# Optimization experiments

Hardware: AMD Instinct MI355X
Metric: run time of the kernel (lower is better)

Reference implementation:

```python
import jax, jax.numpy as jnp
import numpy as np

GROUP = 128  # int4 quant group size and Hadamard block size

# Sylvester Hadamard matrix of size 128, orthonormal (H @ H.T = I)
_h = np.array([[1.0]], dtype=np.float32)
while _h.shape[0] < GROUP:
    _h = np.kron(_h, np.array([[1.0, 1.0], [1.0, -1.0]], dtype=np.float32))
H128 = jnp.asarray(_h / np.sqrt(GROUP))


def hadamard_rotate(x):
    # blockwise Hadamard rotation along the last dim (last dim % 128 == 0)
    *lead, n = x.shape
    xr = x.reshape(*lead, n // GROUP, GROUP) @ H128
    return xr.reshape(*lead, n)


def dequant_int4(wq, scales):
    # wq: [out, in] uint4 values in [0,16); scales: [out, in//GROUP]
    out_dim, in_dim = wq.shape
    w = (wq.astype(jnp.float32) - 8.0).reshape(out_dim, in_dim // GROUP, GROUP)
    w = w * scales[:, :, None]
    return w.reshape(out_dim, in_dim)


def rotate_linear_int4(x, wq, scales):
    # y = hadamard(x) @ dequant(W).T
    return hadamard_rotate(x) @ dequant_int4(wq, scales).T


def setup_inputs() -> dict:
    key = jax.random.key(0)
    ks = jax.random.split(key, 7)
    T, D, I = 4096, 4096, 12288  # tokens, hidden, intermediate
    x = jax.random.normal(ks[0], (T, D), dtype=jnp.float32)
    wq_gate = jax.random.randint(ks[1], (I, D), 0, 16, dtype=jnp.int32)
    s_gate = jax.random.uniform(ks[2], (I, D // GROUP), dtype=jnp.float32) * 0.01
    wq_up = jax.random.randint(ks[3], (I, D), 0, 16, dtype=jnp.int32)
    s_up = jax.random.uniform(ks[4], (I, D // GROUP), dtype=jnp.float32) * 0.01
    wq_down = jax.random.randint(ks[5], (D, I), 0, 16, dtype=jnp.int32)
    s_down = jax.random.uniform(ks[6], (D, I // GROUP), dtype=jnp.float32) * 0.01
    return {"x": x, "wq_gate": wq_gate, "s_gate": s_gate,
            "wq_up": wq_up, "s_up": s_up,
            "wq_down": wq_down, "s_down": s_down}


def reference(x, wq_gate, s_gate, wq_up, s_up, wq_down, s_down):
    gate = rotate_linear_int4(x, wq_gate, s_gate)   # [T, I]
    up = rotate_linear_int4(x, wq_up, s_up)         # [T, I]
    h = jax.nn.silu(gate) * up                       # SiluAndMul on cat([gate, up])
    return rotate_linear_int4(h, wq_down, s_down)    # [T, D]
```

## Files before the change

kernel.cpp:

```cpp
#include <hip/hip_runtime.h>
#include <hip/hip_bf16.h>
#include <cstdint>

#define T_DIM 4096
#define D_DIM 4096
#define I_DIM 12288
#define GRP   128

typedef __attribute__((ext_vector_type(8))) short bf16x8;
typedef __attribute__((ext_vector_type(4))) float f32x4;
typedef __attribute__((ext_vector_type(4))) int   int32x4;

typedef __attribute__((address_space(3))) void lds_void;
typedef const __attribute__((address_space(1))) void gmem_void;

static __device__ __forceinline__ unsigned short f2bf(float f) {
    unsigned int u = __float_as_uint(f);
    u += 0x7FFFu + ((u >> 16) & 1u);
    return (unsigned short)(u >> 16);
}
static __device__ __forceinline__ float bf2f(unsigned short b) {
    return __uint_as_float(((unsigned int)b) << 16);
}

__global__ void had_f32_to_bf16(const float* __restrict__ in, unsigned short* __restrict__ out,
                                int ngroups) {
    int gid = blockIdx.x * (blockDim.x >> 6) + (threadIdx.x >> 6);
    if (gid >= ngroups) return;
    int lane = threadIdx.x & 63;
    const float2 v2 = *reinterpret_cast<const float2*>(in + (size_t)gid * 128 + lane * 2);
    float v0 = v2.x, v1 = v2.y;
    { float t0 = v0 + v1, t1 = v0 - v1; v0 = t0; v1 = t1; }
#pragma unroll
    for (int m = 1; m <= 32; m <<= 1) {
        float b0 = __shfl_xor(v0, m);
        float b1 = __shfl_xor(v1, m);
        if (lane & m) { v0 = b0 - v0; v1 = b1 - v1; }
        else          { v0 = v0 + b0; v1 = v1 + b1; }
    }
    const float s = 0.08838834764831843f;
    unsigned int o = (unsigned int)f2bf(v0 * s) | ((unsigned int)f2bf(v1 * s) << 16);
    *reinterpret_cast<unsigned int*>(out + (size_t)gid * 128 + lane * 2) = o;
}

__global__ void had_bf16_inplace(unsigned short* __restrict__ buf, int ngroups) {
    int gid = blockIdx.x * (blockDim.x >> 6) + (threadIdx.x >> 6);
    if (gid >= ngroups) return;
    int lane = threadIdx.x & 63;
    unsigned int pv = *reinterpret_cast<const unsigned int*>(buf + (size_t)gid * 128 + lane * 2);
    float v0 = __uint_as_float((pv & 0xFFFFu) << 16);
    float v1 = __uint_as_float(pv & 0xFFFF0000u);
    { float t0 = v0 + v1, t1 = v0 - v1; v0 = t0; v1 = t1; }
#pragma unroll
    for (int m = 1; m <= 32; m <<= 1) {
        float b0 = __shfl_xor(v0, m);
        float b1 = __shfl_xor(v1, m);
        if (lane & m) { v0 = b0 - v0; v1 = b1 - v1; }
        else          { v0 = v0 + b0; v1 = v1 + b1; }
    }
    const float s = 0.08838834764831843f;
    unsigned int o = (unsigned int)f2bf(v0 * s) | ((unsigned int)f2bf(v1 * s) << 16);
    *reinterpret_cast<unsigned int*>(buf + (size_t)gid * 128 + lane * 2) = o;
}

__global__ void dequant_w(const int* __restrict__ Wq, const float* __restrict__ S,
                          unsigned short* __restrict__ Wbf, int In, int total8) {
    int t = blockIdx.x * blockDim.x + threadIdx.x;
    if (t >= total8) return;
    size_t base = (size_t)t * 8;
    size_t row = base / (size_t)In;
    int col = (int)(base - row * (size_t)In);
    float sc = S[row * (size_t)(In >> 7) + (col >> 7)];
    const int32x4* p = reinterpret_cast<const int32x4*>(Wq + base);
    int32x4 a = p[0], b = p[1];
    float nsc = -8.0f * sc;
    unsigned int o0 = (unsigned int)f2bf((float)a.x * sc + nsc) |
                      ((unsigned int)f2bf((float)a.y * sc + nsc) << 16);
    unsigned int o1 = (unsigned int)f2bf((float)a.z * sc + nsc) |
                      ((unsigned int)f2bf((float)a.w * sc + nsc) << 16);
    unsigned int o2 = (unsigned int)f2bf((float)b.x * sc + nsc) |
                      ((unsigned int)f2bf((float)b.y * sc + nsc) << 16);
    unsigned int o3 = (unsigned int)f2bf((float)b.z * sc + nsc) |
                      ((unsigned int)f2bf((float)b.w * sc + nsc) << 16);
    *reinterpret_cast<uint4*>(Wbf + base) = make_uint4(o0, o1, o2, o3);
}


#define GBAR()  __builtin_amdgcn_s_barrier()
#define LGKM0() asm volatile("s_waitcnt lgkmcnt(0)" ::: "memory")
#define VM4()   asm volatile("s_waitcnt vmcnt(4)" ::: "memory")
#define VM0()   asm volatile("s_waitcnt vmcnt(0)" ::: "memory")

#define STAGE(bb, s, kb)                                                               \
  { const int kh_ = (s) >> 1;                                                          \
    const unsigned short* src_ = ((s) & 1) ? W : A;                                    \
    const int row0_ = ((s) & 1) ? n0 : m0;                                             \
    _Pragma("unroll")                                                                  \
    for (int i_ = 0; i_ < 2; ++i_) {                                                   \
      int j_ = i_ * 512 + tid;                                                         \
      int row_ = j_ >> 2;                                                              \
      int gs_ = (tid & 3) ^ ((row_ >> 1) & 3);                                         \
      const unsigned short* gp_ = src_ + (size_t)(row0_ + row_) * K + (kb) + kh_ * 32 + gs_ * 8; \
      unsigned short* lp_ = lds + ((bb) << 15) + (((s) & 1) << 14) + (kh_ << 13)       \
                            + (i_ * 512 + (wid << 6)) * 8;                             \
      __builtin_amdgcn_global_load_lds((gmem_void*)gp_, (lds_void*)lp_, 16, 0, 0);     \
    } }

#define LOADA(bb, kh, mg)                                                              \
  _Pragma("unroll")                                                                    \
  for (int mi_ = 0; mi_ < 4; ++mi_) {                                                  \
    int row_ = (wr << 7) + ((mg) * 4 + mi_) * 16 + (lane & 15);                        \
    af[mi_] = *reinterpret_cast<const bf16x8*>(lds + ((bb) << 15) + ((kh) << 13)       \
              + row_ * 32 + ((kc ^ ((row_ >> 1) & 3)) << 3));                          \
  }

#define LOADB(bb, kh)                                                                  \
  _Pragma("unroll")                                                                    \
  for (int ni_ = 0; ni_ < 4; ++ni_) {                                                  \
    int nr_ = (wc << 6) + ni_ * 16 + (lane & 15);                                      \
    bk[ni_] = *reinterpret_cast<const bf16x8*>(lds + ((bb) << 15) + 16384              \
              + ((kh) << 13) + nr_ * 32 + ((kc ^ ((nr_ >> 1) & 3)) << 3));             \
  }

#define MFMA16(mg)                                                                     \
  _Pragma("unroll")                                                                    \
  for (int mi_ = 0; mi_ < 4; ++mi_)                                                    \
  _Pragma("unroll")                                                                    \
  for (int ni_ = 0; ni_ < 4; ++ni_)                                                    \
    acc[(mg) * 4 + mi_][ni_] =                                                         \
      __builtin_amdgcn_mfma_f32_16x16x32_bf16(af[mi_], bk[ni_], acc[(mg) * 4 + mi_][ni_], 0, 0, 0);

template<int MODE>
__global__ __launch_bounds__(512, 2)
void gemm256(const unsigned short* __restrict__ A,
             const unsigned short* __restrict__ W,
             void* __restrict__ C, int M, int N, int K)
{
    __shared__ __align__(16) unsigned short lds[65536];

    const int MT = M >> 8;
    const int nwg = gridDim.x;
    const int bid = blockIdx.x;
    const int cpx = nwg >> 3;
    const int wg  = (bid & 7) * cpx + (bid >> 3);
    const int m0 = (wg % MT) << 8;
    const int n0 = (wg / MT) << 8;

    const int tid  = threadIdx.x;
    const int lane = tid & 63;
    const int wid  = tid >> 6;
    const int wr = wid >> 2;
    const int wc = wid & 3;
    const int kc = lane >> 4;

    f32x4 acc[8][4];
#pragma unroll
    for (int i = 0; i < 8; ++i)
#pragma unroll
        for (int j = 0; j < 4; ++j) acc[i][j] = (f32x4)0.0f;

    const int NT = K >> 6;

    STAGE(0, 0, 0); STAGE(0, 1, 0); STAGE(0, 2, 0); STAGE(0, 3, 0);
    VM4();
    GBAR();

    for (int kt = 0; kt < NT; ++kt) {
        const int b  = kt & 1;
        const int kn = (kt + 1) << 6;
        const bool st = (kt + 1 < NT);
        bf16x8 af[4], bk[4];

        LOADB(b, 0); LOADA(b, 0, 0);
        if (st) STAGE(b ^ 1, 0, kn);
        GBAR(); LGKM0();
        __builtin_amdgcn_s_setprio(1); MFMA16(0); __builtin_amdgcn_s_setprio(0);
        GBAR();
        LOADA(b, 0, 1);
        if (st) STAGE(b ^ 1, 1, kn);
        GBAR(); LGKM0();
        __builtin_amdgcn_s_setprio(1); MFMA16(1); __builtin_amdgcn_s_setprio(0);
        if (st) { VM4(); } else { VM0(); }
        GBAR();
        LOADB(b, 1); LOADA(b, 1, 0);
        if (st) STAGE(b ^ 1, 2, kn);
        GBAR(); LGKM0();
        __builtin_amdgcn_s_setprio(1); MFMA16(0); __builtin_amdgcn_s_setprio(0);
        GBAR();
        LOADA(b, 1, 1);
        if (st) STAGE(b ^ 1, 3, kn);
        GBAR(); LGKM0();
        __builtin_amdgcn_s_setprio(1); MFMA16(1); __builtin_amdgcn_s_setprio(0);
        if (st) { VM4(); }
        GBAR();
    }

#pragma unroll
    for (int mi = 0; mi < 8; ++mi)
#pragma unroll
        for (int ni = 0; ni < 4; ++ni) {
            const int col = n0 + (wc << 6) + ni * 16 + (lane & 15);
#pragma unroll
            for (int r = 0; r < 4; ++r) {
                const int row = m0 + (wr << 7) + mi * 16 + ((lane >> 4) << 2) + r;
                const size_t idx = (size_t)row * N + col;
                if (MODE == 2) {
                    ((float*)C)[idx] = acc[mi][ni][r];
                } else if (MODE == 0) {
                    ((unsigned short*)C)[idx] = f2bf(acc[mi][ni][r]);
                } else {
                    float g = bf2f(((unsigned short*)C)[idx]);
                    float u = acc[mi][ni][r];
                    float h = (g / (1.0f + __expf(-g))) * u;
                    ((unsigned short*)C)[idx] = f2bf(h);
                }
            }
        }
}

__global__ __launch_bounds__(256, 2)
void gemm_gateup_fb(const unsigned short* __restrict__ Xr,
                    const int* __restrict__ Wg, const float* __restrict__ Sg,
                    const int* __restrict__ Wu, const float* __restrict__ Su,
                    unsigned short* __restrict__ H)
{
    __shared__ __align__(16) unsigned short lA [128 * 64];
    __shared__ __align__(16) unsigned short lBg[128 * 64];
    __shared__ __align__(16) unsigned short lBu[128 * 64];
    const int MT = T_DIM / 128;
    const int bid = blockIdx.x;
    const int m0 = (bid % MT) * 128;
    const int n0 = (bid / MT) * 128;
    const int tid  = threadIdx.x;
    const int lane = tid & 63;
    const int wid  = tid >> 6;
    const int wr = wid >> 1, wc = wid & 1;
    f32x4 accG[4][4], accU[4][4];
#pragma unroll
    for (int i = 0; i < 4; ++i)
#pragma unroll
        for (int j = 0; j < 4; ++j) { accG[i][j] = (f32x4)0.0f; accU[i][j] = (f32x4)0.0f; }
    const int arow = lane >> 3;
    const int acol = (lane & 7) * 8;
    const int SStride = D_DIM / GRP;
    for (int k0 = 0; k0 < D_DIM; k0 += 64) {
        __syncthreads();
#pragma unroll
        for (int it = 0; it < 4; ++it) {
            int chunk = wid * 4 + it;
            const unsigned short* gp = Xr + (size_t)(m0 + chunk * 8 + arow) * D_DIM + k0 + acol;
            __builtin_amdgcn_global_load_lds((gmem_void*)gp, (lds_void*)(lA + chunk * 512), 16, 0, 0);
        }
        const int g = k0 >> 7;
#pragma unroll
        for (int i = 0; i < 8; ++i) {
            int linear = i * 1024 + tid * 4;
            int r = linear >> 6;
            int c = linear & 63;
            const int32x4 wg = *reinterpret_cast<const int32x4*>(Wg + (size_t)(n0 + r) * D_DIM + k0 + c);
            const int32x4 wu = *reinterpret_cast<const int32x4*>(Wu + (size_t)(n0 + r) * D_DIM + k0 + c);
            float scg = Sg[(size_t)(n0 + r) * SStride + g];
            float scu = Su[(size_t)(n0 + r) * SStride + g];
            unsigned int g01 = (unsigned int)f2bf((float)(wg.x - 8) * scg) | ((unsigned int)f2bf((float)(wg.y - 8) * scg) << 16);
            unsigned int g23 = (unsigned int)f2bf((float)(wg.z - 8) * scg) | ((unsigned int)f2bf((float)(wg.w - 8) * scg) << 16);
            unsigned int u01 = (unsigned int)f2bf((float)(wu.x - 8) * scu) | ((unsigned int)f2bf((float)(wu.y - 8) * scu) << 16);
            unsigned int u23 = (unsigned int)f2bf((float)(wu.z - 8) * scu) | ((unsigned int)f2bf((float)(wu.w - 8) * scu) << 16);
            *reinterpret_cast<uint2*>(lBg + r * 64 + c) = make_uint2(g01, g23);
            *reinterpret_cast<uint2*>(lBu + r * 64 + c) = make_uint2(u01, u23);
        }
        __syncthreads();
#pragma unroll
        for (int ks = 0; ks < 2; ++ks) {
            const int koff = ks * 32 + (lane >> 4) * 8;
            bf16x8 af[4], bg[4], bu[4];
#pragma unroll
            for (int mi = 0; mi < 4; ++mi)
                af[mi] = *reinterpret_cast<const bf16x8*>(lA + (wr * 64 + mi * 16 + (lane & 15)) * 64 + koff);
#pragma unroll
            for (int ni = 0; ni < 4; ++ni) {
                bg[ni] = *reinterpret_cast<const bf16x8*>(lBg + (wc * 64 + ni * 16 + (lane & 15)) * 64 + koff);
                bu[ni] = *reinterpret_cast<const bf16x8*>(lBu + (wc * 64 + ni * 16 + (lane & 15)) * 64 + koff);
            }
#pragma unroll
            for (int mi = 0; mi < 4; ++mi)
#pragma unroll
                for (int ni = 0; ni < 4; ++ni) {
                    accG[mi][ni] = __builtin_amdgcn_mfma_f32_16x16x32_bf16(af[mi], bg[ni], accG[mi][ni], 0, 0, 0);
                    accU[mi][ni] = __builtin_amdgcn_mfma_f32_16x16x32_bf16(af[mi], bu[ni], accU[mi][ni], 0, 0, 0);
                }
        }
    }
#pragma unroll
    for (int mi = 0; mi < 4; ++mi)
#pragma unroll
        for (int ni = 0; ni < 4; ++ni) {
            const int col = n0 + wc * 64 + ni * 16 + (lane & 15);
#pragma unroll
            for (int r = 0; r < 4; ++r) {
                const int row = m0 + wr * 64 + mi * 16 + (lane >> 4) * 4 + r;
                float gv = accG[mi][ni][r];
                float uv = accU[mi][ni][r];
                float hv = (gv / (1.0f + __expf(-gv))) * uv;
                H[(size_t)row * I_DIM + col] = f2bf(hv);
            }
        }
}

__global__ __launch_bounds__(256, 2)
void gemm_down_fb(const unsigned short* __restrict__ Hr,
                  const int* __restrict__ Wd, const float* __restrict__ Sd,
                  float* __restrict__ Out)
{
    __shared__ __align__(16) unsigned short lA[128 * 64];
    __shared__ __align__(16) unsigned short lB[128 * 64];
    const int MT = T_DIM / 128;
    const int bid = blockIdx.x;
    const int m0 = (bid % MT) * 128;
    const int n0 = (bid / MT) * 128;
    const int tid  = threadIdx.x;
    const int lane = tid & 63;
    const int wid  = tid >> 6;
    const int wr = wid >> 1, wc = wid & 1;
    f32x4 acc[4][4];
#pragma unroll
    for (int i = 0; i < 4; ++i)
#pragma unroll
        for (int j = 0; j < 4; ++j) acc[i][j] = (f32x4)0.0f;
    const int arow = lane >> 3;
    const int acol = (lane & 7) * 8;
    const int SStride = I_DIM / GRP;
    for (int k0 = 0; k0 < I_DIM; k0 += 64) {
        __syncthreads();
#pragma unroll
        for (int it = 0; it < 4; ++it) {
            int chunk = wid * 4 + it;
            const unsigned short* gp = Hr + (size_t)(m0 + chunk * 8 + arow) * I_DIM + k0 + acol;
            __builtin_amdgcn_global_load_lds((gmem_void*)gp, (lds_void*)(lA + chunk * 512), 16, 0, 0);
        }
        const int g = k0 >> 7;
#pragma unroll
        for (int i = 0; i < 8; ++i) {
            int linear = i * 1024 + tid * 4;
            int r = linear >> 6;
            int c = linear & 63;
            const int32x4 wd = *reinterpret_cast<const int32x4*>(Wd + (size_t)(n0 + r) * I_DIM + k0 + c);
            float sc = Sd[(size_t)(n0 + r) * SStride + g];
            unsigned int d01 = (unsigned int)f2bf((float)(wd.x - 8) * sc) | ((unsigned int)f2bf((float)(wd.y - 8) * sc) << 16);
            unsigned int d23 = (unsigned int)f2bf((float)(wd.z - 8) * sc) | ((unsigned int)f2bf((float)(wd.w - 8) * sc) << 16);
            *reinterpret_cast<uint2*>(lB + r * 64 + c) = make_uint2(d01, d23);
        }
        __syncthreads();
#pragma unroll
        for (int ks = 0; ks < 2; ++ks) {
            const int koff = ks * 32 + (lane >> 4) * 8;
            bf16x8 af[4], bfr[4];
#pragma unroll
            for (int mi = 0; mi < 4; ++mi)
                af[mi] = *reinterpret_cast<const bf16x8*>(lA + (wr * 64 + mi * 16 + (lane & 15)) * 64 + koff);
#pragma unroll
            for (int ni = 0; ni < 4; ++ni)
                bfr[ni] = *reinterpret_cast<const bf16x8*>(lB + (wc * 64 + ni * 16 + (lane & 15)) * 64 + koff);
#pragma unroll
            for (int mi = 0; mi < 4; ++mi)
#pragma unroll
                for (int ni = 0; ni < 4; ++ni)
                    acc[mi][ni] = __builtin_amdgcn_mfma_f32_16x16x32_bf16(af[mi], bfr[ni], acc[mi][ni], 0, 0, 0);
        }
    }
#pragma unroll
    for (int mi = 0; mi < 4; ++mi)
#pragma unroll
        for (int ni = 0; ni < 4; ++ni) {
            const int col = n0 + wc * 64 + ni * 16 + (lane & 15);
#pragma unroll
            for (int r = 0; r < 4; ++r) {
                const int row = m0 + wr * 64 + mi * 16 + (lane >> 4) * 4 + r;
                Out[(size_t)row * D_DIM + col] = acc[mi][ni][r];
            }
        }
}

extern "C" void kernel_launch(void* const* d_in, const int* in_sizes, int n_in,
                              void* d_out, int out_size, void* d_ws, size_t ws_size,
                              hipStream_t stream) {
    const float* x       = (const float*)d_in[0];
    const int*   wq_gate = (const int*)d_in[1];
    const float* s_gate  = (const float*)d_in[2];
    const int*   wq_up   = (const int*)d_in[3];
    const float* s_up    = (const float*)d_in[4];
    const int*   wq_down = (const int*)d_in[5];
    const float* s_down  = (const float*)d_in[6];
    float* out = (float*)d_out;

    const size_t XR_E = (size_t)T_DIM * D_DIM;
    const size_t H_E  = (size_t)T_DIM * I_DIM;
    const size_t W_E  = (size_t)I_DIM * D_DIM;
    const size_t need = (XR_E + H_E + 2 * W_E) * sizeof(unsigned short);

    unsigned short* xr = (unsigned short*)d_ws;
    unsigned short* h  = xr + XR_E;

    {
        int ngroups = (int)(XR_E / 128);
        had_f32_to_bf16<<<dim3(ngroups / 4), dim3(256), 0, stream>>>(x, xr, ngroups);
    }

    if (ws_size >= need) {
        unsigned short* wgbf = h + H_E;
        unsigned short* wubf = wgbf + W_E;
        int total8 = (int)(W_E / 8);
        dequant_w<<<dim3((total8 + 255) / 256), dim3(256), 0, stream>>>(wq_gate, s_gate, wgbf, D_DIM, total8);
        dequant_w<<<dim3((total8 + 255) / 256), dim3(256), 0, stream>>>(wq_up,   s_up,   wubf, D_DIM, total8);
        gemm256<0><<<dim3((T_DIM / 256) * (I_DIM / 256)), dim3(512), 0, stream>>>(
            xr, wgbf, (void*)h, T_DIM, I_DIM, D_DIM);
        gemm256<1><<<dim3((T_DIM / 256) * (I_DIM / 256)), dim3(512), 0, stream>>>(
            xr, wubf, (void*)h, T_DIM, I_DIM, D_DIM);
        {
            int ngroups = (int)(H_E / 128);
            had_bf16_inplace<<<dim3(ngroups / 4), dim3(256), 0, stream>>>(h, ngroups);
        }
        dequant_w<<<dim3((total8 + 255) / 256), dim3(256), 0, stream>>>(wq_down, s_down, wgbf, I_DIM, total8);
        gemm256<2><<<dim3((T_DIM / 256) * (D_DIM / 256)), dim3(512), 0, stream>>>(
            h, wgbf, (void*)out, T_DIM, D_DIM, I_DIM);
    } else {
        gemm_gateup_fb<<<dim3((T_DIM / 128) * (I_DIM / 128)), dim3(256), 0, stream>>>(
            xr, wq_gate, s_gate, wq_up, s_up, h);
        {
            int ngroups = (int)(H_E / 128);
            had_bf16_inplace<<<dim3(ngroups / 4), dim3(256), 0, stream>>>(h, ngroups);
        }
        gemm_down_fb<<<dim3((T_DIM / 128) * (D_DIM / 128)), dim3(256), 0, stream>>>(
            h, wq_down, s_down, out);
    }
}
```

Before: 1.415 ms.

## Restructure GEMM mainloop into 8-phase pipeline with full-width 64-K LDS rows

Changes the LDS tile layout from two 32-wide K halves to a single 64-wide row with an 8-way XOR swizzle. The mainloop is rewritten as an 8-phase schedule per two K tiles: B fragments are loaded once per tile and A in four quarter steps, with staging of the next tiles interleaved at finer granularity. The intent is to hide global-to-LDS loads better and cut LDS read traffic for B. It adds more barriers per tile and a hand-tuned vmcnt sequence that assumes NT is even.

Measured after the change: 1.280 ms. 1.11x faster.

```diff
diff --git a/kernel.cpp b/kernel.cpp
--- a/kernel.cpp
+++ b/kernel.cpp
@@ -88,47 +88,53 @@
 
 #define GBAR()  __builtin_amdgcn_s_barrier()
 #define LGKM0() asm volatile("s_waitcnt lgkmcnt(0)" ::: "memory")
-#define VM4()   asm volatile("s_waitcnt vmcnt(4)" ::: "memory")
-#define VM0()   asm volatile("s_waitcnt vmcnt(0)" ::: "memory")
-
-#define STAGE(bb, s, kb)                                                               \
-  { const int kh_ = (s) >> 1;                                                          \
-    const unsigned short* src_ = ((s) & 1) ? W : A;                                    \
-    const int row0_ = ((s) & 1) ? n0 : m0;                                             \
-    _Pragma("unroll")                                                                  \
+#define VMW(n)  asm volatile("s_waitcnt vmcnt(" #n ")" ::: "memory")
+#define P1()    __builtin_amdgcn_s_setprio(1)
+#define P0()    __builtin_amdgcn_s_setprio(0)
+
+#define STG(bb, mat, h, kb)                                                            \
+  { _Pragma("unroll")                                                                  \
     for (int i_ = 0; i_ < 2; ++i_) {                                                   \
-      int j_ = i_ * 512 + tid;                                                         \
-      int row_ = j_ >> 2;                                                              \
-      int gs_ = (tid & 3) ^ ((row_ >> 1) & 3);                                         \
-      const unsigned short* gp_ = src_ + (size_t)(row0_ + row_) * K + (kb) + kh_ * 32 + gs_ * 8; \
-      unsigned short* lp_ = lds + ((bb) << 15) + (((s) & 1) << 14) + (kh_ << 13)       \
-                            + (i_ * 512 + (wid << 6)) * 8;                             \
+      const int rl_ = (h) * 128 + i_ * 64 + (tid >> 3);                                \
+      const int gs_ = (tid & 7) ^ ((tid >> 3) & 7);                                    \
+      const unsigned short* gp_ = ((mat) ? W : A) +                                    \
+          (size_t)(((mat) ? n0 : m0) + rl_) * K + (kb) + gs_ * 8;                      \
+      unsigned short* lp_ = lds + (bb) * 32768 + (mat) * 16384 +                       \
+          ((h) * 128 + i_ * 64 + wid * 8) * 64;                                        \
       __builtin_amdgcn_global_load_lds((gmem_void*)gp_, (lds_void*)lp_, 16, 0, 0);     \
     } }
 
-#define LOADA(bb, kh, mg)                                                              \
-  _Pragma("unroll")                                                                    \
-  for (int mi_ = 0; mi_ < 4; ++mi_) {                                                  \
-    int row_ = (wr << 7) + ((mg) * 4 + mi_) * 16 + (lane & 15);                        \
-    af[mi_] = *reinterpret_cast<const bf16x8*>(lds + ((bb) << 15) + ((kh) << 13)       \
-              + row_ * 32 + ((kc ^ ((row_ >> 1) & 3)) << 3));                          \
+#define LDA(bb, q)                                                                     \
+  _Pragma("unroll")                                                                    \
+  for (int mi_ = 0; mi_ < 2; ++mi_)                                                    \
+  _Pragma("unroll")                                                                    \
+  for (int ks_ = 0; ks_ < 2; ++ks_) {                                                  \
+    int r_ = wr * 128 + ((q) * 2 + mi_) * 16 + (lane & 15);                            \
+    int c_ = ks_ * 4 + kc;                                                             \
+    af[mi_][ks_] = *reinterpret_cast<const bf16x8*>(                                   \
+        lds + (bb) * 32768 + r_ * 64 + ((c_ ^ (r_ & 7)) << 3));                        \
   }
 
-#define LOADB(bb, kh)                                                                  \
-  _Pragma("unroll")                                                                    \
-  for (int ni_ = 0; ni_ < 4; ++ni_) {                                                  \
-    int nr_ = (wc << 6) + ni_ * 16 + (lane & 15);                                      \
-    bk[ni_] = *reinterpret_cast<const bf16x8*>(lds + ((bb) << 15) + 16384              \
-              + ((kh) << 13) + nr_ * 32 + ((kc ^ ((nr_ >> 1) & 3)) << 3));             \
+#define LDB(bb)                                                                        \
+  _Pragma("unroll")                                                                    \
+  for (int ni_ = 0; ni_ < 4; ++ni_)                                                    \
+  _Pragma("unroll")                                                                    \
+  for (int ks_ = 0; ks_ < 2; ++ks_) {                                                  \
+    int r_ = wc * 64 + ni_ * 16 + (lane & 15);                                         \
+    int c_ = ks_ * 4 + kc;                                                             \
+    bk[ni_][ks_] = *reinterpret_cast<const bf16x8*>(                                   \
+        lds + (bb) * 32768 + 16384 + r_ * 64 + ((c_ ^ (r_ & 7)) << 3));                \
   }
 
-#define MFMA16(mg)                                                                     \
-  _Pragma("unroll")                                                                    \
-  for (int mi_ = 0; mi_ < 4; ++mi_)                                                    \
+#define MF16(q)                                                                        \
+  _Pragma("unroll")                                                                    \
+  for (int ks_ = 0; ks_ < 2; ++ks_)                                                    \
+  _Pragma("unroll")                                                                    \
+  for (int mi_ = 0; mi_ < 2; ++mi_)                                                    \
   _Pragma("unroll")                                                                    \
   for (int ni_ = 0; ni_ < 4; ++ni_)                                                    \
-    acc[(mg) * 4 + mi_][ni_] =                                                         \
-      __builtin_amdgcn_mfma_f32_16x16x32_bf16(af[mi_], bk[ni_], acc[(mg) * 4 + mi_][ni_], 0, 0, 0);
+    acc[(q) * 2 + mi_][ni_] = __builtin_amdgcn_mfma_f32_16x16x32_bf16(                 \
+        af[mi_][ks_], bk[ni_][ks_], acc[(q) * 2 + mi_][ni_], 0, 0, 0);
 
 template<int MODE>
 __global__ __launch_bounds__(512, 2)
@@ -160,39 +166,56 @@
         for (int j = 0; j < 4; ++j) acc[i][j] = (f32x4)0.0f;
 
     const int NT = K >> 6;
-
-    STAGE(0, 0, 0); STAGE(0, 1, 0); STAGE(0, 2, 0); STAGE(0, 3, 0);
-    VM4();
+    const int J  = NT >> 1;
+
+    STG(0, 0, 0, 0); STG(0, 0, 1, 0); STG(0, 1, 0, 0); STG(0, 1, 1, 0);
+    STG(1, 1, 0, 64); STG(1, 1, 1, 64);
+    VMW(4);
     GBAR();
 
-    for (int kt = 0; kt < NT; ++kt) {
-        const int b  = kt & 1;
-        const int kn = (kt + 1) << 6;
-        const bool st = (kt + 1 < NT);
-        bf16x8 af[4], bk[4];
-
-        LOADB(b, 0); LOADA(b, 0, 0);
-        if (st) STAGE(b ^ 1, 0, kn);
-        GBAR(); LGKM0();
-        __builtin_amdgcn_s_setprio(1); MFMA16(0); __builtin_amdgcn_s_setprio(0);
-        GBAR();
-        LOADA(b, 0, 1);
-        if (st) STAGE(b ^ 1, 1, kn);
-        GBAR(); LGKM0();
-        __builtin_amdgcn_s_setprio(1); MFMA16(1); __builtin_amdgcn_s_setprio(0);
-        if (st) { VM4(); } else { VM0(); }
-        GBAR();
-        LOADB(b, 1); LOADA(b, 1, 0);
-        if (st) STAGE(b ^ 1, 2, kn);
-        GBAR(); LGKM0();
-        __builtin_amdgcn_s_setprio(1); MFMA16(0); __builtin_amdgcn_s_setprio(0);
-        GBAR();
-        LOADA(b, 1, 1);
-        if (st) STAGE(b ^ 1, 3, kn);
-        GBAR(); LGKM0();
-        __builtin_amdgcn_s_setprio(1); MFMA16(1); __builtin_amdgcn_s_setprio(0);
-        if (st) { VM4(); }
-        GBAR();
+    bf16x8 af[2][2], bk[4][2];
+
+    for (int j = 0; j < J - 1; ++j) {
+        const int ka  = (j << 7);
+        const int kb1 = ka + 64;
+        const int ka2 = ka + 128;
+        const int ka3 = ka + 192;
+        LDB(0); LDA(0, 0); STG(1, 0, 0, kb1);
+        GBAR(); LGKM0(); P1(); MF16(0); P0(); GBAR();
+        LDA(0, 1); STG(1, 0, 1, kb1);
+        GBAR(); LGKM0(); P1(); MF16(1); P0(); GBAR();
+        LDA(0, 2); STG(0, 1, 0, ka2);
+        GBAR(); LGKM0(); P1(); MF16(2); P0(); GBAR();
+        LDA(0, 3); STG(0, 1, 1, ka2);
+        GBAR(); LGKM0(); P1(); MF16(3); P0(); VMW(4); GBAR();
+        LDB(1); LDA(1, 0); STG(0, 0, 0, ka2);
+        GBAR(); LGKM0(); P1(); MF16(0); P0(); GBAR();
+        LDA(1, 1); STG(0, 0, 1, ka2);
+        GBAR(); LGKM0(); P1(); MF16(1); P0(); GBAR();
+        LDA(1, 2); STG(1, 1, 0, ka3);
+        GBAR(); LGKM0(); P1(); MF16(2); P0(); GBAR();
+        LDA(1, 3); STG(1, 1, 1, ka3);
+        GBAR(); LGKM0(); P1(); MF16(3); P0(); VMW(4); GBAR();
+    }
+
+    {
+        const int kb1 = ((NT - 1) << 6);
+        LDB(0); LDA(0, 0); STG(1, 0, 0, kb1);
+        GBAR(); LGKM0(); P1(); MF16(0); P0(); GBAR();
+        LDA(0, 1); STG(1, 0, 1, kb1);
+        GBAR(); LGKM0(); P1(); MF16(1); P0(); GBAR();
+        LDA(0, 2);
+        GBAR(); LGKM0(); P1(); MF16(2); P0(); GBAR();
+        LDA(0, 3);
+        GBAR(); LGKM0(); P1(); MF16(3); P0(); VMW(0); GBAR();
+        LDB(1); LDA(1, 0);
+        GBAR(); LGKM0(); P1(); MF16(0); P0(); GBAR();
+        LDA(1, 1);
+        GBAR(); LGKM0(); P1(); MF16(1); P0(); GBAR();
+        LDA(1, 2);
+        GBAR(); LGKM0(); P1(); MF16(2); P0(); GBAR();
+        LDA(1, 3);
+        GBAR(); LGKM0(); P1(); MF16(3); P0(); GBAR();
     }
 
 #pragma unroll
```

## Replace 256x256 GEMM tile with simpler 128x128 double-buffered tile

Applied to the files above, without the earlier changes.

Replaces the 512-thread 256x256 tile GEMM, which had a finely interleaved 4-phase schedule with priority hints, with a 256-thread 128x128 tile kernel. The new kernel uses K-steps of 32, a simple two-buffer prefetch with a full vmcnt(0) wait each iteration, and a smaller LDS footprint so more workgroups can be resident per CU. The aim is higher occupancy and a simpler pipeline. The cost is lower data reuse per tile, twice the global traffic per FLOP, and more barriers per unit of K.

New measurement: 1.922 ms. 1.36x slower.

```diff
diff --git a/kernel.cpp b/kernel.cpp
--- a/kernel.cpp
+++ b/kernel.cpp
@@ -87,122 +87,101 @@
 
 
 #define GBAR()  __builtin_amdgcn_s_barrier()
-#define LGKM0() asm volatile("s_waitcnt lgkmcnt(0)" ::: "memory")
-#define VM4()   asm volatile("s_waitcnt vmcnt(4)" ::: "memory")
-#define VM0()   asm volatile("s_waitcnt vmcnt(0)" ::: "memory")
-
-#define STAGE(bb, s, kb)                                                               \
-  { const int kh_ = (s) >> 1;                                                          \
-    const unsigned short* src_ = ((s) & 1) ? W : A;                                    \
-    const int row0_ = ((s) & 1) ? n0 : m0;                                             \
-    _Pragma("unroll")                                                                  \
-    for (int i_ = 0; i_ < 2; ++i_) {                                                   \
-      int j_ = i_ * 512 + tid;                                                         \
-      int row_ = j_ >> 2;                                                              \
-      int gs_ = (tid & 3) ^ ((row_ >> 1) & 3);                                         \
-      const unsigned short* gp_ = src_ + (size_t)(row0_ + row_) * K + (kb) + kh_ * 32 + gs_ * 8; \
-      unsigned short* lp_ = lds + ((bb) << 15) + (((s) & 1) << 14) + (kh_ << 13)       \
-                            + (i_ * 512 + (wid << 6)) * 8;                             \
+#define VMW0()  asm volatile("s_waitcnt vmcnt(0)" ::: "memory")
+
+#define STG128(src, row0, bb, matoff, kb)                                              \
+  { _Pragma("unroll")                                                                  \
+    for (int l_ = 0; l_ < 2; ++l_) {                                                   \
+      const int r_ = (wid * 2 + l_) * 16 + (lane >> 2);                                \
+      const int cg_ = (lane & 3) ^ ((r_ >> 1) & 3);                                    \
+      const unsigned short* gp_ = (src) + (size_t)((row0) + r_) * K + (kb) + cg_ * 8;  \
+      unsigned short* lp_ = lds + (bb) * 8192 + (matoff) + (wid * 2 + l_) * 512;       \
       __builtin_amdgcn_global_load_lds((gmem_void*)gp_, (lds_void*)lp_, 16, 0, 0);     \
     } }
 
-#define LOADA(bb, kh, mg)                                                              \
+#define LDA128(bb)                                                                     \
   _Pragma("unroll")                                                                    \
   for (int mi_ = 0; mi_ < 4; ++mi_) {                                                  \
-    int row_ = (wr << 7) + ((mg) * 4 + mi_) * 16 + (lane & 15);                        \
-    af[mi_] = *reinterpret_cast<const bf16x8*>(lds + ((bb) << 15) + ((kh) << 13)       \
-              + row_ * 32 + ((kc ^ ((row_ >> 1) & 3)) << 3));                          \
+    int r_ = wr * 64 + mi_ * 16 + (lane & 15);                                         \
+    af[mi_] = *reinterpret_cast<const bf16x8*>((const char*)lds + (bb) * 16384         \
+              + r_ * 64 + ((kc ^ ((r_ >> 1) & 3)) << 4));                              \
   }
 
-#define LOADB(bb, kh)                                                                  \
+#define LDB128(bb)                                                                     \
   _Pragma("unroll")                                                                    \
   for (int ni_ = 0; ni_ < 4; ++ni_) {                                                  \
-    int nr_ = (wc << 6) + ni_ * 16 + (lane & 15);                                      \
-    bk[ni_] = *reinterpret_cast<const bf16x8*>(lds + ((bb) << 15) + 16384              \
-              + ((kh) << 13) + nr_ * 32 + ((kc ^ ((nr_ >> 1) & 3)) << 3));             \
+    int r_ = wc * 64 + ni_ * 16 + (lane & 15);                                         \
+    bf[ni_] = *reinterpret_cast<const bf16x8*>((const char*)lds + (bb) * 16384 + 8192  \
+              + r_ * 64 + ((kc ^ ((r_ >> 1) & 3)) << 4));                              \
   }
 
-#define MFMA16(mg)                                                                     \
+#define MF16X()                                                                        \
   _Pragma("unroll")                                                                    \
   for (int mi_ = 0; mi_ < 4; ++mi_)                                                    \
   _Pragma("unroll")                                                                    \
   for (int ni_ = 0; ni_ < 4; ++ni_)                                                    \
-    acc[(mg) * 4 + mi_][ni_] =                                                         \
-      __builtin_amdgcn_mfma_f32_16x16x32_bf16(af[mi_], bk[ni_], acc[(mg) * 4 + mi_][ni_], 0, 0, 0);
+    acc[mi_][ni_] = __builtin_amdgcn_mfma_f32_16x16x32_bf16(                           \
+        af[mi_], bf[ni_], acc[mi_][ni_], 0, 0, 0);
 
 template<int MODE>
-__global__ __launch_bounds__(512, 2)
-void gemm256(const unsigned short* __restrict__ A,
+__global__ __launch_bounds__(256, 4)
+void gemm128(const unsigned short* __restrict__ A,
              const unsigned short* __restrict__ W,
              void* __restrict__ C, int M, int N, int K)
 {
-    __shared__ __align__(16) unsigned short lds[65536];
-
-    const int MT = M >> 8;
+    __shared__ __align__(16) unsigned short lds[16384];
+
+    const int MT = M >> 7;
     const int nwg = gridDim.x;
     const int bid = blockIdx.x;
     const int cpx = nwg >> 3;
     const int wg  = (bid & 7) * cpx + (bid >> 3);
-    const int m0 = (wg % MT) << 8;
-    const int n0 = (wg / MT) << 8;
+    const int m0 = (wg % MT) << 7;
+    const int n0 = (wg / MT) << 7;
 
     const int tid  = threadIdx.x;
     const int lane = tid & 63;
     const int wid  = tid >> 6;
-    const int wr = wid >> 2;
-    const int wc = wid & 3;
+    const int wr = wid >> 1;
+    const int wc = wid & 1;
     const int kc = lane >> 4;
 
-    f32x4 acc[8][4];
-#pragma unroll
-    for (int i = 0; i < 8; ++i)
+    f32x4 acc[4][4];
+#pragma unroll
+    for (int i = 0; i < 4; ++i)
 #pragma unroll
         for (int j = 0; j < 4; ++j) acc[i][j] = (f32x4)0.0f;
 
-    const int NT = K >> 6;
-
-    STAGE(0, 0, 0); STAGE(0, 1, 0); STAGE(0, 2, 0); STAGE(0, 3, 0);
-    VM4();
+    const int NT = K >> 5;
+
+    bf16x8 af[4], bf[4];
+
+    STG128(A, m0, 0, 0, 0);
+    STG128(W, n0, 0, 4096, 0);
+    VMW0();
     GBAR();
 
-    for (int kt = 0; kt < NT; ++kt) {
-        const int b  = kt & 1;
-        const int kn = (kt + 1) << 6;
-        const bool st = (kt + 1 < NT);
-        bf16x8 af[4], bk[4];
-
-        LOADB(b, 0); LOADA(b, 0, 0);
-        if (st) STAGE(b ^ 1, 0, kn);
-        GBAR(); LGKM0();
-        __builtin_amdgcn_s_setprio(1); MFMA16(0); __builtin_amdgcn_s_setprio(0);
+    for (int t = 0; t < NT; ++t) {
+        const int bb = t & 1;
+        if (t + 1 < NT) {
+            const int kn = (t + 1) << 5;
+            STG128(A, m0, bb ^ 1, 0, kn);
+            STG128(W, n0, bb ^ 1, 4096, kn);
+        }
+        LDA128(bb); LDB128(bb);
+        MF16X();
+        VMW0();
         GBAR();
-        LOADA(b, 0, 1);
-        if (st) STAGE(b ^ 1, 1, kn);
-        GBAR(); LGKM0();
-        __builtin_amdgcn_s_setprio(1); MFMA16(1); __builtin_amdgcn_s_setprio(0);
-        if (st) { VM4(); } else { VM0(); }
-        GBAR();
-        LOADB(b, 1); LOADA(b, 1, 0);
-        if (st) STAGE(b ^ 1, 2, kn);
-        GBAR(); LGKM0();
-        __builtin_amdgcn_s_setprio(1); MFMA16(0); __builtin_amdgcn_s_setprio(0);
-        GBAR();
-        LOADA(b, 1, 1);
-        if (st) STAGE(b ^ 1, 3, kn);
-        GBAR(); LGKM0();
-        __builtin_amdgcn_s_setprio(1); MFMA16(1); __builtin_amdgcn_s_setprio(0);
-        if (st) { VM4(); }
-        GBAR();
-    }
-
-#pragma unroll
-    for (int mi = 0; mi < 8; ++mi)
+    }
+
+#pragma unroll
+    for (int mi = 0; mi < 4; ++mi)
 #pragma unroll
         for (int ni = 0; ni < 4; ++ni) {
-            const int col = n0 + (wc << 6) + ni * 16 + (lane & 15);
+            const int col = n0 + wc * 64 + ni * 16 + (lane & 15);
 #pragma unroll
             for (int r = 0; r < 4; ++r) {
-                const int row = m0 + (wr << 7) + mi * 16 + ((lane >> 4) << 2) + r;
+                const int row = m0 + wr * 64 + mi * 16 + ((lane >> 4) << 2) + r;
                 const size_t idx = (size_t)row * N + col;
                 if (MODE == 2) {
                     ((float*)C)[idx] = acc[mi][ni][r];
@@ -411,16 +390,16 @@
         int total8 = (int)(W_E / 8);
         dequant_w<<<dim3((total8 + 255) / 256), dim3(256), 0, stream>>>(wq_gate, s_gate, wgbf, D_DIM, total8);
         dequant_w<<<dim3((total8 + 255) / 256), dim3(256), 0, stream>>>(wq_up,   s_up,   wubf, D_DIM, total8);
-        gemm256<0><<<dim3((T_DIM / 256) * (I_DIM / 256)), dim3(512), 0, stream>>>(
+        gemm128<0><<<dim3((T_DIM / 128) * (I_DIM / 128)), dim3(256), 0, stream>>>(
             xr, wgbf, (void*)h, T_DIM, I_DIM, D_DIM);
-        gemm256<1><<<dim3((T_DIM / 256) * (I_DIM / 256)), dim3(512), 0, stream>>>(
+        gemm128<1><<<dim3((T_DIM / 128) * (I_DIM / 128)), dim3(256), 0, stream>>>(
             xr, wubf, (void*)h, T_DIM, I_DIM, D_DIM);
         {
             int ngroups = (int)(H_E / 128);
             had_bf16_inplace<<<dim3(ngroups / 4), dim3(256), 0, stream>>>(h, ngroups);
         }
         dequant_w<<<dim3((total8 + 255) / 256), dim3(256), 0, stream>>>(wq_down, s_down, wgbf, I_DIM, total8);
-        gemm256<2><<<dim3((T_DIM / 256) * (D_DIM / 256)), dim3(512), 0, stream>>>(
+        gemm128<2><<<dim3((T_DIM / 128) * (D_DIM / 128)), dim3(256), 0, stream>>>(
             h, wgbf, (void*)out, T_DIM, D_DIM, I_DIM);
     } else {
         gemm_gateup_fb<<<dim3((T_DIM / 128) * (I_DIM / 128)), dim3(256), 0, stream>>>(
```
